# Kernel tuning notes

Hardware: AMD Instinct MI355X
Metric: run time of the kernel (lower is better)

## Reference

```python
import jax, jax.numpy as jnp
import numpy as np
from jax import lax

# Surrogate spike: forward = Heaviside, backward = g / (1 + 5|x|)^2
@jax.custom_vjp
def spike_fn(x):
    return (x >= 0).astype(x.dtype)

def _spk_fwd(x):
    return spike_fn(x), x

def _spk_bwd(x, g):
    return (g / (1.0 + 5.0 * jnp.abs(x)) ** 2,)

spike_fn.defvjp(_spk_fwd, _spk_bwd)

BN_EPS = 1e-5

def _batchnorm(x, scale, bias, mean, var):
    # x: (B, C, T); eval-mode BN with running stats
    inv = scale / jnp.sqrt(var + BN_EPS)
    return x * inv[None, :, None] + (bias - mean * inv)[None, :, None]

def _conv1d(x, w, b, pad):
    y = lax.conv_general_dilated(x, w, (1,), [(pad, pad)],
                                 dimension_numbers=('NCH', 'OIH', 'NCH'))
    return y + b[None, :, None]

def setup_inputs() -> dict:
    key = jax.random.key(0)
    ks = jax.random.split(key, 12)
    B, T, EEG, GEO, TH, H, OUT = 4096, 320, 64, 18, 32, 16, 4
    inp = {
        'x_eeg': jax.random.normal(ks[0], (B, T, EEG), jnp.float32),
        'x_geo': jax.random.normal(ks[1], (B, T, GEO), jnp.float32),
        'conv1_w': jax.random.normal(ks[2], (TH, EEG, 5), jnp.float32) * 0.05,
        'conv1_b': jnp.zeros((TH,), jnp.float32),
        'bn1_s': jnp.ones((TH,), jnp.float32),
        'bn1_b': jnp.zeros((TH,), jnp.float32),
        'bn1_m': jnp.zeros((TH,), jnp.float32),
        'bn1_v': jnp.ones((TH,), jnp.float32),
        'conv2_w': jax.random.normal(ks[3], (H, TH, 3), jnp.float32) * 0.1,
        'conv2_b': jnp.zeros((H,), jnp.float32),
        'bn2_s': jnp.ones((H,), jnp.float32),
        'bn2_b': jnp.zeros((H,), jnp.float32),
        'bn2_m': jnp.zeros((H,), jnp.float32),
        'bn2_v': jnp.ones((H,), jnp.float32),
        'geo_w': jax.random.normal(ks[4], (H, GEO), jnp.float32) * 0.2,
        'geo_b': jnp.zeros((H,), jnp.float32),
        'gamma': jnp.full((H,), 0.5, jnp.float32),
        'fc1_w': jax.random.normal(ks[5], (64, 160), jnp.float32) * 0.08,
        'fc1_b': jnp.zeros((64,), jnp.float32),
        'fc2_w': jax.random.normal(ks[6], (OUT, 64), jnp.float32) * 0.12,
        'fc2_b': jnp.zeros((OUT,), jnp.float32),
    }
    return inp

def reference(x_eeg, x_geo, conv1_w, conv1_b, bn1_s, bn1_b, bn1_m, bn1_v,
              conv2_w, conv2_b, bn2_s, bn2_b, bn2_m, bn2_v,
              geo_w, geo_b, gamma, fc1_w, fc1_b, fc2_w, fc2_b):
    B, T, _ = x_eeg.shape
    theta_0, beta, tau_a, tau_m = 0.5, 1.8, 0.36, 0.8

    # EEG temporal encoder (eval mode: dropout = identity)
    h = x_eeg.transpose(0, 2, 1)  # (B, 64, T)
    h = jax.nn.relu(_batchnorm(_conv1d(h, conv1_w, conv1_b, 2), bn1_s, bn1_b, bn1_m, bn1_v))
    h = jax.nn.relu(_batchnorm(_conv1d(h, conv2_w, conv2_b, 1), bn2_s, bn2_b, bn2_m, bn2_v))
    eeg_encoded = h.transpose(0, 2, 1)  # (B, T, 16)

    geo_mod = jax.nn.sigmoid(jnp.einsum('bti,hi->bth', x_geo, geo_w) + geo_b)  # (B, T, 16)

    H = eeg_encoded.shape[-1]
    zeros = jnp.zeros((B, H), x_eeg.dtype)
    init = (zeros, zeros, zeros, zeros)  # mem_alif, eta, mem_li, prev_spk

    def step(carry, xs):
        mem_alif, eta, mem_li, prev_spk = carry
        cur_eeg, cur_geo = xs
        eta = tau_a * eta + (1.0 - tau_a) * prev_spk
        theta_t = theta_0 + beta * eta - gamma * cur_geo
        mem_alif = tau_m * mem_alif + cur_eeg
        spk = spike_fn(mem_alif - theta_t)
        mem_alif = mem_alif * (1.0 - spk)
        mem_li = 0.9 * mem_li + spk
        return (mem_alif, eta, mem_li, spk), mem_li

    xs = (eeg_encoded.transpose(1, 0, 2), geo_mod.transpose(1, 0, 2))  # (T, B, 16)
    _, pot = lax.scan(step, init, xs)  # (T, B, 16)

    pot = pot.transpose(1, 2, 0)                 # (B, 16, T)
    windows = pot.reshape(B, H, 10, 32)          # T = 320 = 10*32
    dp_feat = (windows[..., 16:].mean(-1) - windows[..., :16].mean(-1)).reshape(B, -1)  # (B, 160)

    out = jax.nn.relu(dp_feat @ fc1_w.T + fc1_b) @ fc2_w.T + fc2_b  # (B, 4)
    return out
```

## Files before the change

kernel.cpp:

```cpp
#include <hip/hip_runtime.h>
#include <math.h>

#define TB    4096
#define TSEQ  320
#define NEEG  64
#define NTH   32
#define NH    16
#define NGEO  18
#define TILE_T 64
#define NTILES 5

typedef _Float16 f16x8 __attribute__((ext_vector_type(8)));
typedef _Float16 f16x2 __attribute__((ext_vector_type(2)));
typedef float f32x4 __attribute__((ext_vector_type(4)));
#define INV2048 4.8828125e-4f

#define OFF_W1F  0
#define OFF_W2F  10240
#define OFF_B1   11776
#define OFF_B2   11808
#define OFF_GWT  11824
#define OFF_FC1T 12112
#define OFF_FC2T 22352
#define OFF_ZP   22656
#define OFF_E    32768
#define SZ_EC    (TB*TSEQ*NH)
#define OFF_C    (OFF_E + SZ_EC)
#define OFF_DP   (OFF_C + SZ_EC)
#define SZ_DP    (TB*160)
#define REQ_FLOATS ((size_t)OFF_DP + SZ_DP)
#define REQ_BYTES  (REQ_FLOATS * 4)

__global__ void __launch_bounds__(256)
prep_kernel(const float* __restrict__ c1w, const float* __restrict__ c1b,
            const float* __restrict__ s1,  const float* __restrict__ bb1,
            const float* __restrict__ mm1, const float* __restrict__ vv1,
            const float* __restrict__ c2w, const float* __restrict__ c2b,
            const float* __restrict__ s2,  const float* __restrict__ bb2,
            const float* __restrict__ mm2, const float* __restrict__ vv2,
            const float* __restrict__ gw,  const float* __restrict__ fc1w,
            const float* __restrict__ fc2w, float* __restrict__ ws)
{
    const int tid = threadIdx.x;
    _Float16* w1fp = reinterpret_cast<_Float16*>(ws + OFF_W1F);
    _Float16* w2fp = reinterpret_cast<_Float16*>(ws + OFF_W2F);

    for (int d = tid; d < 10240; d += 256) {
        int j = d & 7, l = (d >> 3) & 63, nbk = d >> 9;
        int kk = nbk >> 1, nb = nbk & 1;
        int k = kk >> 1, i = (kk & 1) * 32 + ((l >> 4) * 8) + j;
        int c = nb * 16 + (l & 15);
        float inv = s1[c] / sqrtf(vv1[c] + 1e-5f);
        float wv = c1w[c * 320 + i * 5 + k] * inv;
        _Float16 hi = (_Float16)wv;
        _Float16 lo = (_Float16)((wv - (float)hi) * 2048.f);
        w1fp[((nbk * 2 + 0) * 64 + l) * 8 + j] = hi;
        w1fp[((nbk * 2 + 1) * 64 + l) * 8 + j] = lo;
    }
    for (int d = tid; d < 1536; d += 256) {
        int j = d & 7, l = (d >> 3) & 63, kk2 = d >> 9;
        int c = (l >> 4) * 8 + j;
        int o = l & 15;
        float inv = s2[o] / sqrtf(vv2[o] + 1e-5f);
        float wv = c2w[o * 96 + c * 3 + kk2] * inv;
        _Float16 hi = (_Float16)wv;
        _Float16 lo = (_Float16)((wv - (float)hi) * 2048.f);
        w2fp[((kk2 * 2 + 0) * 64 + l) * 8 + j] = hi;
        w2fp[((kk2 * 2 + 1) * 64 + l) * 8 + j] = lo;
    }
    if (tid < NTH) {
        float inv = s1[tid] / sqrtf(vv1[tid] + 1e-5f);
        ws[OFF_B1 + tid] = c1b[tid] * inv + bb1[tid] - mm1[tid] * inv;
    }
    if (tid < NH) {
        float inv = s2[tid] / sqrtf(vv2[tid] + 1e-5f);
        ws[OFF_B2 + tid] = c2b[tid] * inv + bb2[tid] - mm2[tid] * inv;
    }
    for (int d = tid; d < NGEO * NH; d += 256) {
        int i = d / NH, h = d - i * NH;
        ws[OFF_GWT + d] = gw[h * NGEO + i];
    }
    for (int d = tid; d < 160 * 64; d += 256) {
        int f = d / 64, o = d - f * 64;
        ws[OFF_FC1T + d] = fc1w[o * 160 + f];
    }
    if (tid < 256) {
        int j = tid / 4, o = tid - j * 4;
        ws[OFF_FC2T + tid] = fc2w[o * 64 + j];
    }
    if (tid < 64) ws[OFF_ZP + tid] = 0.f;
}

__global__ void __launch_bounds__(256, 2)
convm_kernel(const float* __restrict__ xeeg, const float* __restrict__ xgeo,
             const float* __restrict__ ws,   const float* __restrict__ geo_b,
             const float* __restrict__ gamma,
             float* __restrict__ E, float* __restrict__ C)
{
    __shared__ __align__(16) float xf32[2][70 * 64];
    __shared__ __align__(16) float xg32[2][18 * 64];
    __shared__ __align__(16) _Float16 xh[70 * 64];
    __shared__ __align__(16) _Float16 xl[70 * 64];
    __shared__ __align__(16) _Float16 h1h[66 * 32];
    __shared__ __align__(16) _Float16 h1l[66 * 32];
    __shared__ __align__(16) float gws[NGEO * NH];
    __shared__ float b1s[32], b2s[16], gbs[16], gams[16];

    const int b = blockIdx.x, tid = threadIdx.x;
    const int l = tid & 63, w = tid >> 6;
    const int lrow = l & 15, lkg = l >> 4;
    const int nb = w >> 1, wsub = w & 1;
    const int ug = tid >> 2, hq = tid & 3;

    const float* xb  = xeeg + (size_t)b * TSEQ * NEEG;
    const float* xgb = xgeo + (size_t)b * TSEQ * NGEO;
    const float* zp  = ws + OFF_ZP;

#define STAGE_DMA(buf, t0n) do {                                                     \
        for (int c_ = w; c_ < 70; c_ += 4) {                                         \
            int tg_ = (t0n) - 3 + c_;                                                \
            const float* s_ = (tg_ >= 0 && tg_ < TSEQ)                               \
                              ? (xb + (size_t)tg_ * 64 + l) : zp;                    \
            __builtin_amdgcn_global_load_lds(                                        \
                (const __attribute__((address_space(1))) void*)s_,                   \
                (__attribute__((address_space(3))) void*)&xf32[(buf)][c_ * 64],      \
                4, 0, 0);                                                            \
        }                                                                            \
        for (int c_ = w; c_ < 18; c_ += 4) {                                         \
            const float* s_ = xgb + (size_t)(t0n) * NGEO + c_ * 64 + l;              \
            __builtin_amdgcn_global_load_lds(                                        \
                (const __attribute__((address_space(1))) void*)s_,                   \
                (__attribute__((address_space(3))) void*)&xg32[(buf)][c_ * 64],      \
                4, 0, 0);                                                            \
        }                                                                            \
    } while (0)

    f16x8 B1h[10], B1l[10], B2h[3], B2l[3];
    {
        const f16x8* wsrc = reinterpret_cast<const f16x8*>(ws + OFF_W1F);
        #pragma unroll
        for (int kk = 0; kk < 10; ++kk) {
            B1h[kk] = wsrc[((kk * 2 + nb) * 2 + 0) * 64 + l];
            B1l[kk] = wsrc[((kk * 2 + nb) * 2 + 1) * 64 + l];
        }
        const f16x8* wsrc2 = reinterpret_cast<const f16x8*>(ws + OFF_W2F);
        #pragma unroll
        for (int kk = 0; kk < 3; ++kk) {
            B2h[kk] = wsrc2[(kk * 2 + 0) * 64 + l];
            B2l[kk] = wsrc2[(kk * 2 + 1) * 64 + l];
        }
    }
    {
        if (tid < 32) b1s[tid] = ws[OFF_B1 + tid];
        if (tid < 16) {
            b2s[tid] = ws[OFF_B2 + tid];
            gbs[tid] = geo_b[tid];
            gams[tid] = gamma[tid];
        }
        for (int p = tid; p < NGEO * NH; p += 256) gws[p] = ws[OFF_GWT + p];
    }
    STAGE_DMA(0, 0);
    __syncthreads();

    for (int jt = 0; jt < NTILES; ++jt) {
        const int t0 = jt * TILE_T;
        const int cur = jt & 1;

        #pragma unroll
        for (int q = 0; q < 9; ++q) {
            int p = tid + q * 256;
            if (p < 2240) {
                int xr = p >> 5, ip = (p & 31) * 2;
                float2 f2 = *reinterpret_cast<const float2*>(&xf32[cur][xr * 64 + ip]);
                _Float16 h0 = (_Float16)f2.x, h1v = (_Float16)f2.y;
                f16x2 vh = {h0, h1v};
                f16x2 vl = {(_Float16)((f2.x - (float)h0) * 2048.f),
                            (_Float16)((f2.y - (float)h1v) * 2048.f)};
                int idx = xr * 64 + (((ip >> 3) ^ (xr & 7)) << 3) + (ip & 7);
                *reinterpret_cast<f16x2*>(&xh[idx]) = vh;
                *reinterpret_cast<f16x2*>(&xl[idx]) = vl;
            }
        }
        __syncthreads();

        if (jt + 1 < NTILES) STAGE_DMA((jt + 1) & 1, (jt + 1) * TILE_T);
        __builtin_amdgcn_s_setprio(1);
        {
            const float bia = b1s[nb * 16 + lrow];
            #pragma unroll
            for (int pi = 0; pi < 3; ++pi) {
                if (pi == 2 && ((jt & 1) != wsub)) break;
                const int mb = (pi < 2) ? (wsub + pi * 2) : 4;
                const int mbase = mb * 16;
                int s = mbase + lrow; if (s > 65) s = 65;
                f32x4 aH = {0.f, 0.f, 0.f, 0.f};
                f32x4 aM = aH, aL = aH;
                #pragma unroll
                for (int kk = 0; kk < 10; ++kk) {
                    const int xr = s + (kk >> 1);
                    const int gx = (kk & 1) * 4 + lkg;
                    const int off = xr * 64 + ((gx ^ (xr & 7)) << 3);
                    f16x8 Ah = *reinterpret_cast<const f16x8*>(&xh[off]);
                    f16x8 Al = *reinterpret_cast<const f16x8*>(&xl[off]);
                    aH = __builtin_amdgcn_mfma_f32_16x16x32_f16(Ah, B1h[kk], aH, 0, 0, 0);
                    aM = __builtin_amdgcn_mfma_f32_16x16x32_f16(Ah, B1l[kk], aM, 0, 0, 0);
                    aL = __builtin_amdgcn_mfma_f32_16x16x32_f16(Al, B1h[kk], aL, 0, 0, 0);
                }
                #pragma unroll
                for (int r = 0; r < 4; ++r) {
                    int so = mbase + lkg * 4 + r;
                    if (so < 66) {
                        int tg = t0 - 1 + so;
                        bool v = (tg >= 0 && tg < TSEQ);
                        float val = v ? fmaxf(fmaf(aM[r] + aL[r], INV2048, aH[r]) + bia, 0.f) : 0.f;
                        int key = (so >> 1) & 3;
                        int g = (nb * 2 + (lrow >> 3)) ^ key;
                        int idx = so * 32 + (g << 3) + (lrow & 7);
                        _Float16 hh = (_Float16)val;
                        h1h[idx] = hh;
                        h1l[idx] = (_Float16)((val - (float)hh) * 2048.f);
                    }
                }
            }
        }
        __builtin_amdgcn_s_setprio(0);
        __syncthreads();

        {
            const int ub = w * 16;
            f32x4 aH = {0.f, 0.f, 0.f, 0.f};
            f32x4 aM = aH, aL = aH;
            __builtin_amdgcn_s_setprio(1);
            #pragma unroll
            for (int kk = 0; kk < 3; ++kk) {
                int srow = ub + lrow + kk;
                int off = srow * 32 + ((lkg ^ ((srow >> 1) & 3)) << 3);
                f16x8 Ah = *reinterpret_cast<const f16x8*>(&h1h[off]);
                f16x8 Al = *reinterpret_cast<const f16x8*>(&h1l[off]);
                aH = __builtin_amdgcn_mfma_f32_16x16x32_f16(Ah, B2h[kk], aH, 0, 0, 0);
                aM = __builtin_amdgcn_mfma_f32_16x16x32_f16(Ah, B2l[kk], aM, 0, 0, 0);
                aL = __builtin_amdgcn_mfma_f32_16x16x32_f16(Al, B2h[kk], aL, 0, 0, 0);
            }
            __builtin_amdgcn_s_setprio(0);
            const float bia = b2s[lrow];
            float4 ev;
            float* evp = reinterpret_cast<float*>(&ev);
            #pragma unroll
            for (int r = 0; r < 4; ++r)
                evp[r] = fmaxf(fmaf(aM[r] + aL[r], INV2048, aH[r]) + bia, 0.f);
            float* ep = E + ((size_t)b * 16 + lrow) * TSEQ + t0 + ub + lkg * 4;
            *reinterpret_cast<float4*>(ep) = ev;
        }
        {
            float z0 = gbs[hq * 4 + 0], z1 = gbs[hq * 4 + 1];
            float z2 = gbs[hq * 4 + 2], z3 = gbs[hq * 4 + 3];
            const float* xgr = &xg32[cur][ug * NGEO];
            #pragma unroll
            for (int ii = 0; ii < NGEO; ++ii) {
                float xv = xgr[ii];
                float4 wv = *reinterpret_cast<const float4*>(&gws[ii * 16 + hq * 4]);
                z0 = fmaf(xv, wv.x, z0);
                z1 = fmaf(xv, wv.y, z1);
                z2 = fmaf(xv, wv.z, z2);
                z3 = fmaf(xv, wv.w, z3);
            }
            const int tcur = t0 + ug;
            C[((size_t)b * 16 + hq * 4 + 0) * TSEQ + tcur] = gams[hq * 4 + 0] * (1.f / (1.f + expf(-z0)));
            C[((size_t)b * 16 + hq * 4 + 1) * TSEQ + tcur] = gams[hq * 4 + 1] * (1.f / (1.f + expf(-z1)));
            C[((size_t)b * 16 + hq * 4 + 2) * TSEQ + tcur] = gams[hq * 4 + 2] * (1.f / (1.f + expf(-z2)));
            C[((size_t)b * 16 + hq * 4 + 3) * TSEQ + tcur] = gams[hq * 4 + 3] * (1.f / (1.f + expf(-z3)));
        }
    }
#undef STAGE_DMA
}

__global__ void __launch_bounds__(256)
scan_kernel(const float* __restrict__ E, const float* __restrict__ C,
            float* __restrict__ DP)
{
    const int tid = threadIdx.x;
    const int h = tid & 15;
    const int b = blockIdx.x * 16 + (tid >> 4);
    const float4* e4 = reinterpret_cast<const float4*>(E) + ((size_t)b * 16 + h) * 80;
    const float4* c4 = reinterpret_cast<const float4*>(C) + ((size_t)b * 16 + h) * 80;

    float eta = 0.f, memv = 0.f, li = 0.f, ps = 0.f, accF = 0.f, accS = 0.f;
    float4 ev = e4[0], cv = c4[0];
    for (int t4 = 0; t4 < 80; ++t4) {
        float4 en, cn;
        if (t4 < 79) { en = e4[t4 + 1]; cn = c4[t4 + 1]; }
        const float* evp = reinterpret_cast<const float*>(&ev);
        const float* cvp = reinterpret_cast<const float*>(&cv);
        #pragma unroll
        for (int tt = 0; tt < 4; ++tt) {
            float e = evp[tt], c = cvp[tt];
            eta = 0.36f * eta + 0.64f * ps;
            float theta = 0.5f + 1.8f * eta - c;
            memv = 0.8f * memv + e;
            float spk = (memv - theta >= 0.f) ? 1.f : 0.f;
            memv *= (1.f - spk);
            li = 0.9f * li + spk;
            ps = spk;
            int t = t4 * 4 + tt;
            if (((t >> 4) & 1) == 0) accF += li; else accS += li;
        }
        if ((t4 & 7) == 7) {
            DP[(size_t)b * 160 + h * 10 + (t4 >> 3)] = (accS - accF) * 0.0625f;
            accF = 0.f; accS = 0.f;
        }
        ev = en; cv = cn;
    }
}

__global__ void __launch_bounds__(256)
fc_kernel(const float* __restrict__ DP, const float* __restrict__ ws,
          const float* __restrict__ fc1_b, const float* __restrict__ fc2_b,
          float* __restrict__ out)
{
    __shared__ float sh_dp[4][160];
    __shared__ float mid[4][64];
    const int tid = threadIdx.x;
    const int b0 = blockIdx.x * 4;
    for (int p = tid; p < 640; p += 256)
        sh_dp[p / 160][p - (p / 160) * 160] = DP[(size_t)b0 * 160 + p];
    __syncthreads();
    {
        const int bl = tid >> 6, o = tid & 63;
        const float* __restrict__ fc1t = ws + OFF_FC1T;
        float z = fc1_b[o];
        for (int f = 0; f < 160; ++f) z = fmaf(sh_dp[bl][f], fc1t[f * 64 + o], z);
        mid[bl][o] = fmaxf(z, 0.f);
    }
    __syncthreads();
    if (tid < 16) {
        const int bl = tid >> 2, oo = tid & 3;
        const float* __restrict__ fc2t = ws + OFF_FC2T;
        float z = fc2_b[oo];
        #pragma unroll
        for (int jj = 0; jj < 64; ++jj) z = fmaf(mid[bl][jj], fc2t[jj * 4 + oo], z);
        out[(size_t)(b0 + bl) * 4 + oo] = z;
    }
}

extern "C" void kernel_launch(void* const* d_in, const int* in_sizes, int n_in,
                              void* d_out, int out_size, void* d_ws, size_t ws_size,
                              hipStream_t stream)
{
    const float* xeeg = (const float*)d_in[0];
    const float* xgeo = (const float*)d_in[1];
    const float* c1w  = (const float*)d_in[2];
    const float* c1b  = (const float*)d_in[3];
    const float* s1   = (const float*)d_in[4];
    const float* bb1  = (const float*)d_in[5];
    const float* mm1  = (const float*)d_in[6];
    const float* vv1  = (const float*)d_in[7];
    const float* c2w  = (const float*)d_in[8];
    const float* c2b  = (const float*)d_in[9];
    const float* s2   = (const float*)d_in[10];
    const float* bb2  = (const float*)d_in[11];
    const float* mm2  = (const float*)d_in[12];
    const float* vv2  = (const float*)d_in[13];
    const float* gw   = (const float*)d_in[14];
    const float* gb   = (const float*)d_in[15];
    const float* gam  = (const float*)d_in[16];
    const float* fc1w = (const float*)d_in[17];
    const float* fc1b = (const float*)d_in[18];
    const float* fc2w = (const float*)d_in[19];
    const float* fc2b = (const float*)d_in[20];
    float* ws   = (float*)d_ws;
    float* outp = (float*)d_out;

    hipLaunchKernelGGL(prep_kernel, dim3(1), dim3(256), 0, stream,
                       c1w, c1b, s1, bb1, mm1, vv1, c2w, c2b, s2, bb2, mm2, vv2,
                       gw, fc1w, fc2w, ws);

    float* E  = ws + OFF_E;
    float* C  = ws + OFF_C;
    float* DP = ws + OFF_DP;
    hipLaunchKernelGGL(convm_kernel, dim3(TB), dim3(256), 0, stream,
                       xeeg, xgeo, ws, gb, gam, E, C);
    hipLaunchKernelGGL(scan_kernel, dim3(TB / 16), dim3(256), 0, stream,
                       E, C, DP);
    hipLaunchKernelGGL(fc_kernel, dim3(TB / 4), dim3(256), 0, stream,
                       DP, ws, fc1b, fc2b, outp);
}
```

Measured before the change: 340.6 us.

## Alias fp16 split buffers onto fp32 staging buffer to raise occupancy

Drops the separate fp16 hi/lo LDS arrays and the second geo buffer. The fp32 tile is read into registers, the geo projection runs early, and after a barrier the hi/lo halves are written back into the same staging buffer. This cuts LDS per block enough to raise launch bounds from 2 to 3 blocks per CU, aiming for better latency hiding. The cost is an extra __syncthreads per tile and 9 float2 values held in registers, which may pressure the register budget at the higher occupancy.

New measurement: 711.8 us. 2.09x slower.

```diff
diff --git a/kernel.cpp b/kernel.cpp
--- a/kernel.cpp
+++ b/kernel.cpp
@@ -91,16 +91,14 @@
     if (tid < 64) ws[OFF_ZP + tid] = 0.f;
 }
 
-__global__ void __launch_bounds__(256, 2)
+__global__ void __launch_bounds__(256, 3)
 convm_kernel(const float* __restrict__ xeeg, const float* __restrict__ xgeo,
              const float* __restrict__ ws,   const float* __restrict__ geo_b,
              const float* __restrict__ gamma,
              float* __restrict__ E, float* __restrict__ C)
 {
-    __shared__ __align__(16) float xf32[2][70 * 64];
-    __shared__ __align__(16) float xg32[2][18 * 64];
-    __shared__ __align__(16) _Float16 xh[70 * 64];
-    __shared__ __align__(16) _Float16 xl[70 * 64];
+    __shared__ __align__(16) float xbuf[2][70 * 64];
+    __shared__ __align__(16) float xg32[18 * 64];
     __shared__ __align__(16) _Float16 h1h[66 * 32];
     __shared__ __align__(16) _Float16 h1l[66 * 32];
     __shared__ __align__(16) float gws[NGEO * NH];
@@ -123,14 +121,14 @@
                               ? (xb + (size_t)tg_ * 64 + l) : zp;                    \
             __builtin_amdgcn_global_load_lds(                                        \
                 (const __attribute__((address_space(1))) void*)s_,                   \
-                (__attribute__((address_space(3))) void*)&xf32[(buf)][c_ * 64],      \
+                (__attribute__((address_space(3))) void*)&xbuf[(buf)][c_ * 64],      \
                 4, 0, 0);                                                            \
         }                                                                            \
         for (int c_ = w; c_ < 18; c_ += 4) {                                         \
             const float* s_ = xgb + (size_t)(t0n) * NGEO + c_ * 64 + l;              \
             __builtin_amdgcn_global_load_lds(                                        \
                 (const __attribute__((address_space(1))) void*)s_,                   \
-                (__attribute__((address_space(3))) void*)&xg32[(buf)][c_ * 64],      \
+                (__attribute__((address_space(3))) void*)&xg32[c_ * 64],             \
                 4, 0, 0);                                                            \
         }                                                                            \
     } while (0)
@@ -165,17 +163,49 @@
     for (int jt = 0; jt < NTILES; ++jt) {
         const int t0 = jt * TILE_T;
         const int cur = jt & 1;
-
+        _Float16* xh = reinterpret_cast<_Float16*>(&xbuf[cur][0]);
+        _Float16* xl = xh + 70 * 64;
+
+        float2 xr2[9];
         #pragma unroll
         for (int q = 0; q < 9; ++q) {
             int p = tid + q * 256;
             if (p < 2240) {
                 int xr = p >> 5, ip = (p & 31) * 2;
-                float2 f2 = *reinterpret_cast<const float2*>(&xf32[cur][xr * 64 + ip]);
-                _Float16 h0 = (_Float16)f2.x, h1v = (_Float16)f2.y;
+                xr2[q] = *reinterpret_cast<const float2*>(&xbuf[cur][xr * 64 + ip]);
+            }
+        }
+        {
+            float z0 = gbs[hq * 4 + 0], z1 = gbs[hq * 4 + 1];
+            float z2 = gbs[hq * 4 + 2], z3 = gbs[hq * 4 + 3];
+            const float* xgr = &xg32[ug * NGEO];
+            #pragma unroll
+            for (int ii = 0; ii < NGEO; ++ii) {
+                float xv = xgr[ii];
+                float4 wv = *reinterpret_cast<const float4*>(&gws[ii * 16 + hq * 4]);
+                z0 = fmaf(xv, wv.x, z0);
+                z1 = fmaf(xv, wv.y, z1);
+                z2 = fmaf(xv, wv.z, z2);
+                z3 = fmaf(xv, wv.w, z3);
+            }
+            const int tcur = t0 + ug;
+            C[((size_t)b * 16 + hq * 4 + 0) * TSEQ + tcur] = gams[hq * 4 + 0] * (1.f / (1.f + expf(-z0)));
+            C[((size_t)b * 16 + hq * 4 + 1) * TSEQ + tcur] = gams[hq * 4 + 1] * (1.f / (1.f + expf(-z1)));
+            C[((size_t)b * 16 + hq * 4 + 2) * TSEQ + tcur] = gams[hq * 4 + 2] * (1.f / (1.f + expf(-z2)));
+            C[((size_t)b * 16 + hq * 4 + 3) * TSEQ + tcur] = gams[hq * 4 + 3] * (1.f / (1.f + expf(-z3)));
+        }
+        __syncthreads();
+
+        #pragma unroll
+        for (int q = 0; q < 9; ++q) {
+            int p = tid + q * 256;
+            if (p < 2240) {
+                int xr = p >> 5, ip = (p & 31) * 2;
+                float f0 = xr2[q].x, f1 = xr2[q].y;
+                _Float16 h0 = (_Float16)f0, h1v = (_Float16)f1;
                 f16x2 vh = {h0, h1v};
-                f16x2 vl = {(_Float16)((f2.x - (float)h0) * 2048.f),
-                            (_Float16)((f2.y - (float)h1v) * 2048.f)};
+                f16x2 vl = {(_Float16)((f0 - (float)h0) * 2048.f),
+                            (_Float16)((f1 - (float)h1v) * 2048.f)};
                 int idx = xr * 64 + (((ip >> 3) ^ (xr & 7)) << 3) + (ip & 7);
                 *reinterpret_cast<f16x2*>(&xh[idx]) = vh;
                 *reinterpret_cast<f16x2*>(&xl[idx]) = vl;
@@ -183,7 +213,7 @@
         }
         __syncthreads();
 
-        if (jt + 1 < NTILES) STAGE_DMA((jt + 1) & 1, (jt + 1) * TILE_T);
+        if (jt + 1 < NTILES) STAGE_DMA(cur ^ 1, (jt + 1) * TILE_T);
         __builtin_amdgcn_s_setprio(1);
         {
             const float bia = b1s[nb * 16 + lrow];
@@ -251,25 +281,6 @@
             float* ep = E + ((size_t)b * 16 + lrow) * TSEQ + t0 + ub + lkg * 4;
             *reinterpret_cast<float4*>(ep) = ev;
         }
-        {
-            float z0 = gbs[hq * 4 + 0], z1 = gbs[hq * 4 + 1];
-            float z2 = gbs[hq * 4 + 2], z3 = gbs[hq * 4 + 3];
-            const float* xgr = &xg32[cur][ug * NGEO];
-            #pragma unroll
-            for (int ii = 0; ii < NGEO; ++ii) {
-                float xv = xgr[ii];
-                float4 wv = *reinterpret_cast<const float4*>(&gws[ii * 16 + hq * 4]);
-                z0 = fmaf(xv, wv.x, z0);
-                z1 = fmaf(xv, wv.y, z1);
-                z2 = fmaf(xv, wv.z, z2);
-                z3 = fmaf(xv, wv.w, z3);
-            }
-            const int tcur = t0 + ug;
-            C[((size_t)b * 16 + hq * 4 + 0) * TSEQ + tcur] = gams[hq * 4 + 0] * (1.f / (1.f + expf(-z0)));
-            C[((size_t)b * 16 + hq * 4 + 1) * TSEQ + tcur] = gams[hq * 4 + 1] * (1.f / (1.f + expf(-z1)));
-            C[((size_t)b * 16 + hq * 4 + 2) * TSEQ + tcur] = gams[hq * 4 + 2] * (1.f / (1.f + expf(-z2)));
-            C[((size_t)b * 16 + hq * 4 + 3) * TSEQ + tcur] = gams[hq * 4 + 3] * (1.f / (1.f + expf(-z3)));
-        }
     }
 #undef STAGE_DMA
 }
```
